# Kernel optimization log

Measured on AMD Instinct MI355X. Metric: run time of the kernel, lower is better.

The kernel has to match this reference:

```python
import jax, jax.numpy as jnp
import numpy as np

BN_EPS = 1e-5


def _bn(x, gamma, beta):
    # x: [B, C, L]; training-mode BatchNorm1d: biased stats over (B, L) per channel.
    mu = x.mean(axis=(0, 2), keepdims=True)
    var = x.var(axis=(0, 2), keepdims=True)
    return (x - mu) * jax.lax.rsqrt(var + BN_EPS) * gamma[None, :, None] + beta[None, :, None]


def _sblock(x, g1, be1, w1, bi1, g2, be2, w2, bi2):
    # x: [B, m, n] (n == m). bn1 over channel dim n after transpose.
    t = jnp.swapaxes(x, -2, -1)                      # [B, n, m]
    t = jax.nn.relu(_bn(t, g1, be1))
    t = jnp.einsum('bnm,km->bnk', t, w1) + bi1       # Linear(n,n) on last dim
    t = jnp.swapaxes(t, -2, -1)                      # [B, m, n]
    t = jax.nn.relu(_bn(t, g2, be2))                 # bn2 over channel dim m
    t = jnp.einsum('bmn,kn->bmk', t, w2) + bi2       # Linear(m,m) on last dim
    return t


def _forward(x, bn1_gamma, bn1_beta, w1, b1, bn2_gamma, bn2_beta, w2, b2):
    out = x
    num_blocks = w1.shape[0]
    for l in range(num_blocks):
        out = _sblock(out, bn1_gamma[l], bn1_beta[l], w1[l], b1[l],
                      bn2_gamma[l], bn2_beta[l], w2[l], b2[l])
    n, m = out.shape[-2], out.shape[-1]

    # greedy argmax row/col masking on a detached copy (batch index 0, as in torch)
    oc0 = jax.lax.stop_gradient(out[0])              # [n, m]
    neg_inf = jnp.float32(-jnp.inf)

    def body(line, state):
        oc, visited, mask = state
        idx = jnp.argmax(oc)
        i, j = idx // m, idx % m
        visited = visited.at[i].set(1.0)
        mask = mask.at[:, j].set(1.0 - visited)
        oc = oc.at[:, j].set(neg_inf)
        oc = oc.at[i, :].set(neg_inf)
        return oc, visited, mask

    init = (oc0, jnp.zeros((n,), jnp.float32), jnp.zeros((n, m), jnp.float32))
    _, _, mask = jax.lax.fori_loop(0, n, body, init)

    out = jnp.where(mask.astype(bool)[None], neg_inf, out)
    return jax.nn.softmax(out, axis=-1)


def setup_inputs() -> dict:
    key = jax.random.key(0)
    ks = jax.random.split(key, 9)
    L, n, m = 2, 2048, 2048
    return {
        'x': jax.random.normal(ks[0], (1, m, n), jnp.float32),
        'bn1_gamma': jax.random.uniform(ks[1], (L, n), jnp.float32, 0.5, 1.5),
        'bn1_beta': 0.1 * jax.random.normal(ks[2], (L, n), jnp.float32),
        'w1': 0.02 * jax.random.normal(ks[3], (L, n, n), jnp.float32),
        'b1': 0.02 * jax.random.normal(ks[4], (L, n), jnp.float32),
        'bn2_gamma': jax.random.uniform(ks[5], (L, m), jnp.float32, 0.5, 1.5),
        'bn2_beta': 0.1 * jax.random.normal(ks[6], (L, m), jnp.float32),
        'w2': 0.02 * jax.random.normal(ks[7], (L, m, m), jnp.float32),
        'b2': 0.02 * jax.random.normal(ks[8], (L, m), jnp.float32),
    }


def reference(x, bn1_gamma, bn1_beta, w1, b1, bn2_gamma, bn2_beta, w2, b2):
    return _forward(x, bn1_gamma, bn1_beta, w1, b1, bn2_gamma, bn2_beta, w2, b2)
```

## Files before the change

### kernel.cpp

```cpp
#include <hip/hip_runtime.h>
#include <math.h>

#define NEG_INF (-__builtin_inf())

typedef unsigned long long u64;

constexpr int N = 2048;
constexpr int NCHUNK = 32;
constexpr int RPC = N / NCHUNK;
constexpr int K_LIST = 64;
constexpr int BCAND = 128;
constexpr int CMAX = 256;
constexpr int CTGT = 96;

template<typename T> struct Key;
template<> struct Key<float>{
  static __device__ inline u64 pack(float x){
    unsigned u = __float_as_uint(x);
    u = (u & 0x80000000u) ? ~u : (u | 0x80000000u);
    return ((u64)u) << 32;
  }
};
template<> struct Key<double>{
  static __device__ inline u64 pack(double x){
    u64 u = (u64)__double_as_longlong(x);
    return (u >> 63) ? ~u : (u | 0x8000000000000000ull);
  }
};

__device__ inline bool kbetter(u64 k, unsigned rc, u64 bk, unsigned brc){
  return (k > bk) || (k == bk && rc < brc);
}

template<typename T>
__global__ __launch_bounds__(256) void colstats_partial(const T* __restrict__ X, double* __restrict__ part){
  int col = blockIdx.x * 256 + threadIdx.x;
  int r0  = blockIdx.y * RPC;
  double s = 0.0, q = 0.0;
  for (int r = r0; r < r0 + RPC; ++r){
    double v = (double)X[(size_t)r * N + col];
    s += v; q += v * v;
  }
  size_t o = (size_t)blockIdx.y * N + col;
  part[o*2+0] = s; part[o*2+1] = q;
}

__global__ __launch_bounds__(256) void colstats_final(const double* __restrict__ part,
    const float* __restrict__ g, const float* __restrict__ be,
    double* __restrict__ A, double* __restrict__ C){
  int col = blockIdx.x * 256 + threadIdx.x;
  double s = 0.0, q = 0.0;
  for (int k = 0; k < NCHUNK; ++k){
    size_t o = (size_t)k * N + col;
    s += part[o*2+0]; q += part[o*2+1];
  }
  double mu  = s / (double)N;
  double var = q / (double)N - mu * mu;
  double inv = 1.0 / sqrt(var + 1e-5);
  double a = (double)g[col] * inv;
  A[col] = a;
  C[col] = (double)be[col] - mu * a;
}

template<typename T>
__global__ __launch_bounds__(256) void rowstats(const T* __restrict__ Z,
    const float* __restrict__ g, const float* __restrict__ be,
    double* __restrict__ A, double* __restrict__ C){
  __shared__ double s1[256], s2[256];
  int r = blockIdx.x, tx = threadIdx.x;
  double s = 0.0, q = 0.0;
  for (int j = tx; j < N; j += 256){
    double v = (double)Z[(size_t)r * N + j];
    s += v; q += v * v;
  }
  s1[tx] = s; s2[tx] = q; __syncthreads();
  for (int st = 128; st; st >>= 1){
    if (tx < st){ s1[tx] += s1[tx + st]; s2[tx] += s2[tx + st]; }
    __syncthreads();
  }
  if (tx == 0){
    double mu  = s1[0] / (double)N;
    double var = s2[0] / (double)N - mu * mu;
    double inv = 1.0 / sqrt(var + 1e-5);
    double a = (double)g[r] * inv;
    A[r] = a;
    C[r] = (double)be[r] - mu * a;
  }
}

template<typename Tin, typename Tout>
__global__ __launch_bounds__(256) void bnrelu_col(const Tin* __restrict__ X,
    const double* __restrict__ A, const double* __restrict__ C, Tout* __restrict__ O){
  int i = blockIdx.x;
  for (int j = threadIdx.x; j < N; j += 256){
    double v = fma((double)X[(size_t)i * N + j], A[j], C[j]);
    O[(size_t)i * N + j] = (Tout)(v > 0.0 ? v : 0.0);
  }
}

template<typename Tin, typename Tout>
__global__ __launch_bounds__(256) void bnrelu_row(const Tin* __restrict__ Z,
    const double* __restrict__ A, const double* __restrict__ C, Tout* __restrict__ O){
  int i = blockIdx.x;
  double a = A[i], c = C[i];
  for (int j = threadIdx.x; j < N; j += 256){
    double v = fma((double)Z[(size_t)i * N + j], a, c);
    O[(size_t)i * N + j] = (Tout)(v > 0.0 ? v : 0.0);
  }
}

template<typename TA, typename TB, typename TO, typename TACC, bool BT, bool BIAS_ROW>
__global__ __launch_bounds__(256) void gemm_t(const TA* __restrict__ A, const TB* __restrict__ B,
    const float* __restrict__ bias, TO* __restrict__ O){
  __shared__ TACC sA[16][68];
  __shared__ TACC sB[16][68];
  const int tid = threadIdx.x;
  const int tx = tid & 15, ty = tid >> 4;
  const int i0 = blockIdx.y * 64, j0 = blockIdx.x * 64;
  TACC acc[4][4] = {};
  for (int k0 = 0; k0 < N; k0 += 16){
    {
      int r = tid >> 2, c4 = (tid & 3) * 4;
      const TA* p = A + (size_t)(i0 + r) * N + k0 + c4;
      TACC v0 = (TACC)p[0], v1 = (TACC)p[1], v2 = (TACC)p[2], v3 = (TACC)p[3];
      sA[c4+0][r] = v0; sA[c4+1][r] = v1; sA[c4+2][r] = v2; sA[c4+3][r] = v3;
    }
    if (!BT){
      int k = tid >> 4, j4 = (tid & 15) * 4;
      const TB* p = B + (size_t)(k0 + k) * N + j0 + j4;
      sB[k][j4+0] = (TACC)p[0]; sB[k][j4+1] = (TACC)p[1];
      sB[k][j4+2] = (TACC)p[2]; sB[k][j4+3] = (TACC)p[3];
    } else {
      int j = tid >> 2, c4 = (tid & 3) * 4;
      const TB* p = B + (size_t)(j0 + j) * N + k0 + c4;
      TACC v0 = (TACC)p[0], v1 = (TACC)p[1], v2 = (TACC)p[2], v3 = (TACC)p[3];
      sB[c4+0][j] = v0; sB[c4+1][j] = v1; sB[c4+2][j] = v2; sB[c4+3][j] = v3;
    }
    __syncthreads();
    #pragma unroll
    for (int kk = 0; kk < 16; ++kk){
      TACC a_[4], b_[4];
      #pragma unroll
      for (int q = 0; q < 4; ++q){ a_[q] = sA[kk][ty*4+q]; b_[q] = sB[kk][tx*4+q]; }
      #pragma unroll
      for (int mi = 0; mi < 4; ++mi)
        #pragma unroll
        for (int ni = 0; ni < 4; ++ni)
          acc[mi][ni] = fma(a_[mi], b_[ni], acc[mi][ni]);
    }
    __syncthreads();
  }
  #pragma unroll
  for (int mi = 0; mi < 4; ++mi){
    int i = i0 + ty*4 + mi;
    #pragma unroll
    for (int ni = 0; ni < 4; ++ni){
      int j = j0 + tx*4 + ni;
      TACC bv = BIAS_ROW ? (TACC)bias[i] : (TACC)bias[j];
      O[(size_t)i * N + j] = (TO)(acc[mi][ni] + bv);
    }
  }
}

template<typename T>
__global__ __launch_bounds__(256) void build_lists(const T* __restrict__ O,
    ulonglong2* __restrict__ list, unsigned short* __restrict__ llen,
    u64* __restrict__ rvK_g, unsigned* __restrict__ rvRC_g){
  __shared__ unsigned hist4[4][256];
  __shared__ unsigned hsum[256];
  __shared__ u64 candK[BCAND];
  __shared__ unsigned candRC[BCAND];
  __shared__ u64 redK[256];
  __shared__ unsigned redC[256];
  __shared__ u64 sTau;
  __shared__ unsigned sBstar, sPre, sDone, sC;
  const int r = blockIdx.x;
  const int tid = threadIdx.x;
  const int wave = tid >> 6, lane = tid & 63;
  const unsigned BIG = 0xFFFFFFFFu;
  const T* __restrict__ row = O + (size_t)r * N;
  const unsigned target = K_LIST;

  u64 base = 0; unsigned pre = 0; int shift = 56;
  for (int level = 0; level < 8; ++level){
    for (int i = tid; i < 4*256; i += 256) ((unsigned*)hist4)[i] = 0;
    __syncthreads();
    for (int c = tid; c < N; c += 256){
      u64 k = Key<T>::pack(row[c]);
      if (k >= base && ((k - base) >> shift) < 256)
        atomicAdd(&hist4[wave][(unsigned)((k - base) >> shift)], 1u);
    }
    __syncthreads();
    if (tid < 256) hsum[tid] = hist4[0][tid] + hist4[1][tid] + hist4[2][tid] + hist4[3][tid];
    __syncthreads();
    if (wave == 0){
      unsigned v0 = hsum[4*lane+0], v1 = hsum[4*lane+1], v2 = hsum[4*lane+2], v3 = hsum[4*lane+3];
      unsigned s3 = v3, s2 = v2+v3, s1 = v1+s2, tot = v0+s1;
      unsigned run = tot;
      #pragma unroll
      for (int off = 1; off < 64; off <<= 1){
        unsigned x = __shfl_down(run, off);
        if (lane + off < 64) run += x;
      }
      unsigned above = run - tot;
      unsigned ge0 = tot + above, ge1 = s1 + above, ge2 = s2 + above, ge3 = s3 + above;
      int bl = -1; unsigned geb = 0, vb = 0;
      if (pre + ge3 >= target){ bl = 4*lane+3; geb = ge3; vb = v3; }
      else if (pre + ge2 >= target){ bl = 4*lane+2; geb = ge2; vb = v2; }
      else if (pre + ge1 >= target){ bl = 4*lane+1; geb = ge1; vb = v1; }
      else if (pre + ge0 >= target){ bl = 4*lane+0; geb = ge0; vb = v0; }
      int bmax = bl;
      #pragma unroll
      for (int off = 32; off; off >>= 1){
        int o = __shfl_xor(bmax, off);
        if (o > bmax) bmax = o;
      }
      if (bmax < 0){
        if (lane == 0){ sBstar = 0; sPre = pre; sDone = 1; }
      } else if (bl == bmax){
        unsigned total = pre + geb;
        sBstar = (unsigned)bmax; sPre = pre + geb - vb;
        sDone = (total <= BCAND || shift == 0) ? 1u : 0u;
      }
    }
    __syncthreads();
    unsigned bstar = sBstar;
    if (sDone){
      if (tid == 0) sTau = base + ((u64)bstar << shift);
      break;
    }
    base += ((u64)bstar << shift);
    pre = sPre;
    shift -= 8;
    __syncthreads();
  }
  __syncthreads();
  const u64 tau = sTau;

  if (tid == 0) sC = 0;
  __syncthreads();
  for (int c = tid; c < N; c += 256){
    u64 k = Key<T>::pack(row[c]);
    if (k >= tau){
      unsigned p = atomicAdd(&sC, 1u);
      if (p < BCAND){ candK[p] = k; candRC[p] = ((unsigned)r << 11) | (unsigned)c; }
    }
  }
  __syncthreads();
  unsigned C = sC;

  if (C > BCAND){
    u64 bk = 0; unsigned bc = BIG;
    for (int c = tid; c < N; c += 256){
      u64 k = Key<T>::pack(row[c]);
      if (k > bk){ bk = k; bc = (unsigned)c; }
    }
    redK[tid] = bk; redC[tid] = bc; __syncthreads();
    for (int st = 128; st; st >>= 1){
      if (tid < st && kbetter(redK[tid+st], redC[tid+st], redK[tid], redC[tid])){
        redK[tid] = redK[tid+st]; redC[tid] = redC[tid+st];
      }
      __syncthreads();
    }
    if (tid == 0){
      llen[r] = 0;
      rvK_g[r] = redK[0];
      rvRC_g[r] = ((unsigned)r << 11) | (redC[0] & 2047u);
    }
    return;
  }

  unsigned S = 64; while (S < C) S <<= 1;
  for (unsigned p = C + tid; p < S; p += 256){ candK[p] = 0; candRC[p] = BIG; }
  __syncthreads();
  for (unsigned k2 = 2; k2 <= S; k2 <<= 1){
    for (unsigned jj = k2 >> 1; jj > 0; jj >>= 1){
      if (tid < (int)(S >> 1)){
        unsigned i = (((unsigned)tid & ~(jj - 1)) << 1) | ((unsigned)tid & (jj - 1));
        unsigned l = i | jj;
        bool up = ((i & k2) == 0);
        u64 ki = candK[i], kl = candK[l];
        unsigned ri = candRC[i], rl = candRC[l];
        bool lBeforeI = (kl > ki) || (kl == ki && rl < ri);
        bool iBeforeL = (ki > kl) || (ki == kl && ri < rl);
        if (up ? lBeforeI : iBeforeL){
          candK[i] = kl; candK[l] = ki; candRC[i] = rl; candRC[l] = ri;
        }
      }
      __syncthreads();
    }
  }

  unsigned outLen = (C < (unsigned)K_LIST) ? C : (unsigned)K_LIST;
  if (tid < (int)outLen){
    ulonglong2 e; e.x = candK[tid]; e.y = (u64)candRC[tid];
    list[(size_t)r * K_LIST + tid] = e;
  }
  if (tid == 0){
    llen[r] = (unsigned short)outLen;
    rvK_g[r] = candK[0];
    rvRC_g[r] = candRC[0];
  }
}

template<typename T>
__global__ __launch_bounds__(512) void greedy7(const T* __restrict__ O,
    const ulonglong2* __restrict__ list, const unsigned short* __restrict__ llen_g,
    const u64* __restrict__ rvK_g, const unsigned* __restrict__ rvRC_g,
    unsigned* __restrict__ rowStep_g, unsigned* __restrict__ colStep_g){
  __shared__ u64 rvK[N];
  __shared__ unsigned rvRC[N];
  __shared__ unsigned cm32[N/32];
  __shared__ unsigned short hIdx[N];
  __shared__ unsigned short hLen[N];
  __shared__ unsigned rowStepL[N];
  __shared__ unsigned colStepL[N];
  __shared__ unsigned hist[8][256];
  __shared__ unsigned hsum[256];
  __shared__ u64 candK[CMAX];
  __shared__ unsigned candRC[CMAX];
  __shared__ u64 sortK[CMAX];
  __shared__ unsigned sortRC[CMAX];
  __shared__ unsigned foc[N];
  __shared__ u64 redK8[8];
  __shared__ unsigned redC8[8];
  __shared__ u64 sTau;
  __shared__ unsigned sBstar, sPre, sDone, sC, sCnt, sL;
  const int tid  = threadIdx.x;
  const int lane = tid & 63, wave = tid >> 6;
  const unsigned BIG = 0xFFFFFFFFu;
  const u64 lmask = ((u64)1 << lane) - 1;

  for (int i = tid; i < N; i += 512){
    rvK[i] = rvK_g[i]; rvRC[i] = rvRC_g[i];
    unsigned short L0 = llen_g[i];
    hLen[i] = L0;
    hIdx[i] = (L0 == 0) ? (unsigned short)0xFFFFu : (unsigned short)1;
  }
  if (tid < N/32) cm32[tid] = 0xFFFFFFFFu;
  __syncthreads();

  unsigned t = 0;
  for (int rd = 0; rd < N && t < N; ++rd){
    const unsigned alive = N - t;
    const unsigned target = (alive < (unsigned)CTGT) ? alive : (unsigned)CTGT;
    if (tid == 0){ sC = 0; sCnt = 0; sL = BIG; }

    u64 base = 0; unsigned pre = 0; int shift = 56;
    for (int level = 0; level < 8; ++level){
      for (int i = tid; i < 8*256; i += 512) ((unsigned*)hist)[i] = 0;
      __syncthreads();
      #pragma unroll
      for (int rep = 0; rep < 4; ++rep){
        u64 k = rvK[rep*512 + tid];
        if (k >= base && k && ((k - base) >> shift) < 256)
          atomicAdd(&hist[wave][(unsigned)((k - base) >> shift)], 1u);
      }
      __syncthreads();
      if (tid < 256){
        unsigned s = 0;
        #pragma unroll
        for (int w = 0; w < 8; ++w) s += hist[w][tid];
        hsum[tid] = s;
      }
      __syncthreads();
      if (wave == 0){
        unsigned v0 = hsum[4*lane+0], v1 = hsum[4*lane+1], v2 = hsum[4*lane+2], v3 = hsum[4*lane+3];
        unsigned s3 = v3, s2 = v2+v3, s1 = v1+s2, tot = v0+s1;
        unsigned run = tot;
        #pragma unroll
        for (int off = 1; off < 64; off <<= 1){
          unsigned x = __shfl_down(run, off);
          if (lane + off < 64) run += x;
        }
        unsigned above = run - tot;
        unsigned ge0 = tot + above, ge1 = s1 + above, ge2 = s2 + above, ge3 = s3 + above;
        int bl = -1; unsigned geb = 0, vb = 0;
        if (pre + ge3 >= target){ bl = 4*lane+3; geb = ge3; vb = v3; }
        else if (pre + ge2 >= target){ bl = 4*lane+2; geb = ge2; vb = v2; }
        else if (pre + ge1 >= target){ bl = 4*lane+1; geb = ge1; vb = v1; }
        else if (pre + ge0 >= target){ bl = 4*lane+0; geb = ge0; vb = v0; }
        int bmax = bl;
        #pragma unroll
        for (int off = 32; off; off >>= 1){
          int o = __shfl_xor(bmax, off);
          if (o > bmax) bmax = o;
        }
        if (bmax < 0){
          if (lane == 0){ sBstar = 0; sPre = pre; sDone = 1; }
        } else if (bl == bmax){
          unsigned total = pre + geb;
          sBstar = (unsigned)bmax; sPre = pre + geb - vb;
          sDone = (total <= CMAX || shift == 0) ? 1u : 0u;
        }
      }
      __syncthreads();
      unsigned bstar = sBstar;
      if (sDone){
        if (tid == 0) sTau = base + ((u64)bstar << shift);
        break;
      }
      base += ((u64)bstar << shift);
      pre = sPre;
      shift -= 8;
      __syncthreads();
    }
    __syncthreads();
    const u64 tau = sTau;

    #pragma unroll
    for (int rep = 0; rep < 4; ++rep){
      int i = rep*512 + tid;
      u64 k = rvK[i];
      bool p = (k != 0) && (k >= tau);
      u64 m = __ballot(p);
      unsigned b = 0;
      if (lane == 0) b = atomicAdd(&sC, (unsigned)__popcll(m));
      b = __shfl(b, 0);
      if (p){
        unsigned pos = b + (unsigned)__popcll(m & lmask);
        if (pos < (unsigned)CMAX){ candK[pos] = k; candRC[pos] = rvRC[i]; }
      }
    }
    __syncthreads();
    const unsigned C = sC;

    unsigned L;
    if (C > (unsigned)CMAX){
      u64 bk = 0; unsigned brc = BIG;
      for (int i = tid; i < N; i += 512){
        u64 k = rvK[i];
        if (k && kbetter(k, rvRC[i], bk, brc)){ bk = k; brc = rvRC[i]; }
      }
      #pragma unroll
      for (int off = 32; off; off >>= 1){
        u64 ok = __shfl_xor(bk, off);
        unsigned oc = __shfl_xor(brc, off);
        if (kbetter(ok, oc, bk, brc)){ bk = ok; brc = oc; }
      }
      if (lane == 0){ redK8[wave] = bk; redC8[wave] = brc; }
      __syncthreads();
      if (tid == 0){
        u64 fk = redK8[0]; unsigned fc = redC8[0];
        for (int w = 1; w < 8; ++w)
          if (kbetter(redK8[w], redC8[w], fk, fc)){ fk = redK8[w]; fc = redC8[w]; }
        sortK[0] = fk; sortRC[0] = fc;
      }
      __syncthreads();
      L = 1;
    } else {
      if (tid < (int)C){
        u64 mk = candK[tid]; unsigned mrc = candRC[tid];
        unsigned rank = 0;
        for (unsigned j = 0; j < C; ++j)
          if (kbetter(candK[j], candRC[j], mk, mrc)) ++rank;
        sortK[rank] = mk; sortRC[rank] = mrc;
      }
      __syncthreads();
      if (tid < (int)C) foc[sortRC[tid] & 2047u] = BIG;
      __syncthreads();
      if (tid < (int)C) atomicMin(&foc[sortRC[tid] & 2047u], (unsigned)tid);
      __syncthreads();
      if (tid < (int)C && foc[sortRC[tid] & 2047u] < (unsigned)tid)
        atomicMin(&sL, (unsigned)tid);
      __syncthreads();
      L = (sL < C) ? sL : C;
    }

    if (tid < (int)L){
      unsigned rc = sortRC[tid];
      unsigned r = rc >> 11, c = rc & 2047u;
      rowStepL[r] = t + (unsigned)tid;
      colStepL[c] = t + (unsigned)tid;
      rvK[r] = 0;
      atomicAnd(&cm32[c >> 5], ~(1u << (c & 31)));
    }
    __syncthreads();
    t += L;
    if (t >= N) break;

    #pragma unroll
    for (int rep = 0; rep < 4; ++rep){
      int rr = rep*512 + tid;
      u64 k = rvK[rr];
      if (k == 0) continue;
      unsigned cc = rvRC[rr] & 2047u;
      if ((cm32[cc >> 5] >> (cc & 31)) & 1u) continue;
      unsigned hi = hIdx[rr];
      u64 nk = 0; unsigned nrc = 0;
      if (hi != 0xFFFFu){
        unsigned ln = hLen[rr];
        while (hi < ln){
          ulonglong2 e = list[(size_t)rr * K_LIST + hi];
          ++hi;
          unsigned ec = ((unsigned)e.y) & 2047u;
          if ((cm32[ec >> 5] >> (ec & 31)) & 1u){ nk = e.x; nrc = (unsigned)e.y; break; }
        }
      }
      if (nk){
        rvK[rr] = nk; rvRC[rr] = nrc; hIdx[rr] = (unsigned short)hi;
      } else {
        hIdx[rr] = (unsigned short)0xFFFFu;
        foc[atomicAdd(&sCnt, 1u)] = (unsigned)rr;
      }
    }
    __syncthreads();

    {
      const unsigned cnt = sCnt;
      for (unsigned q = (unsigned)wave; q < cnt; q += 8){
        unsigned rr = foc[q];
        const T* __restrict__ rowp = O + (size_t)rr * N;
        u64 bk = 0; unsigned bc = BIG;
        #pragma unroll
        for (int it = 0; it < N/64; ++it){
          int cc = lane + it*64;
          u64 kk = Key<T>::pack(rowp[cc]);
          if (!((cm32[cc >> 5] >> (cc & 31)) & 1u)) kk = 0;
          if (kbetter(kk, (unsigned)cc, bk, bc)){ bk = kk; bc = (unsigned)cc; }
        }
        #pragma unroll
        for (int off = 32; off; off >>= 1){
          u64 ok = __shfl_xor(bk, off);
          unsigned oc = __shfl_xor(bc, off);
          if (kbetter(ok, oc, bk, bc)){ bk = ok; bc = oc; }
        }
        if (lane == 0){ rvK[rr] = bk; rvRC[rr] = (rr << 11) | (bc & 2047u); }
      }
    }
    __syncthreads();
  }

  __syncthreads();
  for (int i = tid; i < N; i += 512){
    rowStep_g[i] = rowStepL[i];
    colStep_g[i] = colStepL[i];
  }
}

template<typename T>
__global__ __launch_bounds__(256) void masked_softmax(const T* __restrict__ O,
    const unsigned* __restrict__ rowStep, const unsigned* __restrict__ colStep,
    float* __restrict__ out){
  __shared__ double vals[N];
  __shared__ double red[256];
  int r = blockIdx.x, tx = threadIdx.x;
  unsigned s = rowStep[r];
  double mx = NEG_INF;
  for (int c = tx; c < N; c += 256){
    double v = (colStep[c] >= s) ? (double)O[(size_t)r * N + c] : NEG_INF;
    vals[c] = v;
    if (v > mx) mx = v;
  }
  red[tx] = mx; __syncthreads();
  for (int st = 128; st; st >>= 1){
    if (tx < st) red[tx] = fmax(red[tx], red[tx + st]);
    __syncthreads();
  }
  mx = red[0]; __syncthreads();
  double sm = 0.0;
  for (int c = tx; c < N; c += 256){
    double v = vals[c];
    double e = (v != NEG_INF) ? exp(v - mx) : 0.0;
    vals[c] = e;
    sm += e;
  }
  red[tx] = sm; __syncthreads();
  for (int st = 128; st; st >>= 1){
    if (tx < st) red[tx] += red[tx + st];
    __syncthreads();
  }
  double inv = 1.0 / red[0];
  for (int c = tx; c < N; c += 256){
    out[(size_t)r * N + c] = (float)(vals[c] * inv);
  }
}

template<typename T>
static void run_pipeline(const float* x, const float* g1, const float* be1,
                         const float* W1, const float* bi1,
                         const float* g2, const float* be2,
                         const float* W2, const float* bi2,
                         float* out, T* buf0, T* buf1,
                         double* part, double* stA, double* stC,
                         u64* rvK, unsigned* rvRC,
                         unsigned* rowStep, unsigned* colStep,
                         ulonglong2* list, unsigned short* llen,
                         hipStream_t s){
  dim3 gs(N/256, NCHUNK);
  dim3 gg(N/64, N/64);
  colstats_partial<float><<<gs,256,0,s>>>(x, part);
  colstats_final<<<N/256,256,0,s>>>(part, g1, be1, stA, stC);
  bnrelu_col<float,T><<<N,256,0,s>>>(x, stA, stC, buf0);
  gemm_t<float,T,T,T,false,true><<<gg,256,0,s>>>(W1, buf0, bi1, buf1);
  rowstats<T><<<N,256,0,s>>>(buf1, g2, be2, stA, stC);
  bnrelu_row<T,T><<<N,256,0,s>>>(buf1, stA, stC, buf0);
  gemm_t<T,float,T,T,true,false><<<gg,256,0,s>>>(buf0, W2, bi2, buf1);
  colstats_partial<T><<<gs,256,0,s>>>(buf1, part);
  colstats_final<<<N/256,256,0,s>>>(part, g1+N, be1+N, stA, stC);
  bnrelu_col<T,T><<<N,256,0,s>>>(buf1, stA, stC, buf0);
  gemm_t<float,T,T,T,false,true><<<gg,256,0,s>>>(W1+(size_t)N*N, buf0, bi1+N, buf1);
  rowstats<T><<<N,256,0,s>>>(buf1, g2+N, be2+N, stA, stC);
  bnrelu_row<T,T><<<N,256,0,s>>>(buf1, stA, stC, buf0);
  gemm_t<T,float,T,T,true,false><<<gg,256,0,s>>>(buf0, W2+(size_t)N*N, bi2+N, buf1);
  build_lists<T><<<N,256,0,s>>>(buf1, list, llen, rvK, rvRC);
  greedy7<T><<<1,512,0,s>>>(buf1, list, llen, rvK, rvRC, rowStep, colStep);
  masked_softmax<T><<<N,256,0,s>>>(buf1, rowStep, colStep, out);
}

extern "C" void kernel_launch(void* const* d_in, const int* in_sizes, int n_in,
                              void* d_out, int out_size, void* d_ws, size_t ws_size,
                              hipStream_t stream){
  if (n_in < 9) return;
  const float* x   = (const float*)d_in[0];
  const float* g1  = (const float*)d_in[1];
  const float* be1 = (const float*)d_in[2];
  const float* W1  = (const float*)d_in[3];
  const float* bi1 = (const float*)d_in[4];
  const float* g2  = (const float*)d_in[5];
  const float* be2 = (const float*)d_in[6];
  const float* W2  = (const float*)d_in[7];
  const float* bi2 = (const float*)d_in[8];
  float* out = (float*)d_out;

  char* base = (char*)d_ws;
  size_t off = 0;
  auto carve = [&](size_t bytes)->void*{
    void* q = base + off;
    off = (off + bytes + 255) & ~(size_t)255;
    return q;
  };
  double*   part    = (double*)carve((size_t)NCHUNK * N * 2 * sizeof(double));
  double*   stA     = (double*)carve(N * sizeof(double));
  double*   stC     = (double*)carve(N * sizeof(double));
  u64*      rvK     = (u64*)carve(N * sizeof(u64));
  unsigned* rvRC    = (unsigned*)carve(N * sizeof(unsigned));
  unsigned* rowStep = (unsigned*)carve(N * sizeof(unsigned));
  unsigned* colStep = (unsigned*)carve(N * sizeof(unsigned));
  ulonglong2* list  = (ulonglong2*)carve((size_t)N * K_LIST * sizeof(ulonglong2));
  unsigned short* llen = (unsigned short*)carve(N * sizeof(unsigned short));
  size_t smallEnd = off;

  const size_t matF = (size_t)N * N * sizeof(float);
  size_t needF  = smallEnd + 2 * (matF + 256);
  size_t needF1 = smallEnd + 1 * (matF + 256);

  if (ws_size >= needF){
    float* b0 = (float*)carve(matF);
    float* b1 = (float*)carve(matF);
    run_pipeline<float>(x,g1,be1,W1,bi1,g2,be2,W2,bi2, out, b0, b1,
                        part, stA, stC, rvK, rvRC, rowStep, colStep, list, llen, stream);
  } else if (ws_size >= needF1){
    float* b0 = (float*)carve(matF);
    float* b1 = out;
    run_pipeline<float>(x,g1,be1,W1,bi1,g2,be2,W2,bi2, out, b0, b1,
                        part, stA, stC, rvK, rvRC, rowStep, colStep, list, llen, stream);
  }
}
```

Measured before the change: 4.706 ms.

## Keep candidate pool across greedy rounds, rerun radix select only when pool runs low

The single-block greedy matching kernel used to run a full multi-level radix threshold search over all 2048 row maxima every round. It now keeps the sorted candidates that still sit above the previous threshold and whose row value did not change, carries them into the next round, and reruns the radix select only when that pool drops below a minimum size. The radix target is raised so each select yields a larger pool. This is meant to cut the per-round histogram and synchronisation cost in the serial greedy loop. The trade-offs are a larger rank sort per round and added complexity around when pooled candidates remain valid.

```diff
diff --git a/kernel.cpp b/kernel.cpp
--- a/kernel.cpp
+++ b/kernel.cpp
@@ -11,7 +11,8 @@
 constexpr int K_LIST = 64;
 constexpr int BCAND = 128;
 constexpr int CMAX = 256;
-constexpr int CTGT = 96;
+constexpr int CTGT = 240;
+constexpr int POOL_MIN = 48;
 
 template<typename T> struct Key;
 template<> struct Key<float>{
@@ -304,7 +305,7 @@
 }
 
 template<typename T>
-__global__ __launch_bounds__(512) void greedy7(const T* __restrict__ O,
+__global__ __launch_bounds__(512) void greedy9(const T* __restrict__ O,
     const ulonglong2* __restrict__ list, const unsigned short* __restrict__ llen_g,
     const u64* __restrict__ rvK_g, const unsigned* __restrict__ rvRC_g,
     unsigned* __restrict__ rowStep_g, unsigned* __restrict__ colStep_g){
@@ -324,8 +325,8 @@
   __shared__ unsigned foc[N];
   __shared__ u64 redK8[8];
   __shared__ unsigned redC8[8];
-  __shared__ u64 sTau;
-  __shared__ unsigned sBstar, sPre, sDone, sC, sCnt, sL;
+  __shared__ u64 sTau, sTauP;
+  __shared__ unsigned sBstar, sPre, sDone, sC, sCnt, sL, sPC;
   const int tid  = threadIdx.x;
   const int lane = tid & 63, wave = tid >> 6;
   const unsigned BIG = 0xFFFFFFFFu;
@@ -338,95 +339,109 @@
     hIdx[i] = (L0 == 0) ? (unsigned short)0xFFFFu : (unsigned short)1;
   }
   if (tid < N/32) cm32[tid] = 0xFFFFFFFFu;
+  if (tid == 0){ sPC = 0; sTauP = 0; }
   __syncthreads();
 
   unsigned t = 0;
   for (int rd = 0; rd < N && t < N; ++rd){
     const unsigned alive = N - t;
-    const unsigned target = (alive < (unsigned)CTGT) ? alive : (unsigned)CTGT;
-    if (tid == 0){ sC = 0; sCnt = 0; sL = BIG; }
-
-    u64 base = 0; unsigned pre = 0; int shift = 56;
-    for (int level = 0; level < 8; ++level){
-      for (int i = tid; i < 8*256; i += 512) ((unsigned*)hist)[i] = 0;
-      __syncthreads();
+    const unsigned PCin = sPC;
+    const bool needRadix = (PCin < (unsigned)POOL_MIN) && (PCin < alive);
+    if (tid == 0){ sCnt = 0; sL = BIG; }
+
+    unsigned PC;
+    u64 tau;
+    bool overflow = false;
+
+    if (needRadix){
+      const unsigned target = (alive < (unsigned)CTGT) ? alive : (unsigned)CTGT;
+      u64 base = 0; unsigned pre = 0; int shift = 56;
+      for (int level = 0; level < 8; ++level){
+        for (int i = tid; i < 8*256; i += 512) ((unsigned*)hist)[i] = 0;
+        __syncthreads();
+        #pragma unroll
+        for (int rep = 0; rep < 4; ++rep){
+          u64 k = rvK[rep*512 + tid];
+          if (k >= base && k && ((k - base) >> shift) < 256)
+            atomicAdd(&hist[wave][(unsigned)((k - base) >> shift)], 1u);
+        }
+        __syncthreads();
+        if (tid < 256){
+          unsigned s = 0;
+          #pragma unroll
+          for (int w = 0; w < 8; ++w) s += hist[w][tid];
+          hsum[tid] = s;
+        }
+        __syncthreads();
+        if (wave == 0){
+          unsigned v0 = hsum[4*lane+0], v1 = hsum[4*lane+1], v2 = hsum[4*lane+2], v3 = hsum[4*lane+3];
+          unsigned s3 = v3, s2 = v2+v3, s1 = v1+s2, tot = v0+s1;
+          unsigned run = tot;
+          #pragma unroll
+          for (int off = 1; off < 64; off <<= 1){
+            unsigned x = __shfl_down(run, off);
+            if (lane + off < 64) run += x;
+          }
+          unsigned above = run - tot;
+          unsigned ge0 = tot + above, ge1 = s1 + above, ge2 = s2 + above, ge3 = s3 + above;
+          int bl = -1; unsigned geb = 0, vb = 0;
+          if (pre + ge3 >= target){ bl = 4*lane+3; geb = ge3; vb = v3; }
+          else if (pre + ge2 >= target){ bl = 4*lane+2; geb = ge2; vb = v2; }
+          else if (pre + ge1 >= target){ bl = 4*lane+1; geb = ge1; vb = v1; }
+          else if (pre + ge0 >= target){ bl = 4*lane+0; geb = ge0; vb = v0; }
+          int bmax = bl;
+          #pragma unroll
+          for (int off = 32; off; off >>= 1){
+            int o = __shfl_xor(bmax, off);
+            if (o > bmax) bmax = o;
+          }
+          if (bmax < 0){
+            if (lane == 0){ sBstar = 0; sPre = pre; sDone = 1; }
+          } else if (bl == bmax){
+            unsigned total = pre + geb;
+            sBstar = (unsigned)bmax; sPre = pre + geb - vb;
+            sDone = (total <= CMAX || shift == 0) ? 1u : 0u;
+          }
+        }
+        __syncthreads();
+        unsigned bstar = sBstar;
+        if (sDone){
+          if (tid == 0){ sTau = base + ((u64)bstar << shift); sC = 0; }
+          break;
+        }
+        base += ((u64)bstar << shift);
+        pre = sPre;
+        shift -= 8;
+        __syncthreads();
+      }
+      __syncthreads();
+      tau = sTau;
+
       #pragma unroll
       for (int rep = 0; rep < 4; ++rep){
-        u64 k = rvK[rep*512 + tid];
-        if (k >= base && k && ((k - base) >> shift) < 256)
-          atomicAdd(&hist[wave][(unsigned)((k - base) >> shift)], 1u);
-      }
-      __syncthreads();
-      if (tid < 256){
-        unsigned s = 0;
-        #pragma unroll
-        for (int w = 0; w < 8; ++w) s += hist[w][tid];
-        hsum[tid] = s;
-      }
-      __syncthreads();
-      if (wave == 0){
-        unsigned v0 = hsum[4*lane+0], v1 = hsum[4*lane+1], v2 = hsum[4*lane+2], v3 = hsum[4*lane+3];
-        unsigned s3 = v3, s2 = v2+v3, s1 = v1+s2, tot = v0+s1;
-        unsigned run = tot;
-        #pragma unroll
-        for (int off = 1; off < 64; off <<= 1){
-          unsigned x = __shfl_down(run, off);
-          if (lane + off < 64) run += x;
-        }
-        unsigned above = run - tot;
-        unsigned ge0 = tot + above, ge1 = s1 + above, ge2 = s2 + above, ge3 = s3 + above;
-        int bl = -1; unsigned geb = 0, vb = 0;
-        if (pre + ge3 >= target){ bl = 4*lane+3; geb = ge3; vb = v3; }
-        else if (pre + ge2 >= target){ bl = 4*lane+2; geb = ge2; vb = v2; }
-        else if (pre + ge1 >= target){ bl = 4*lane+1; geb = ge1; vb = v1; }
-        else if (pre + ge0 >= target){ bl = 4*lane+0; geb = ge0; vb = v0; }
-        int bmax = bl;
-        #pragma unroll
-        for (int off = 32; off; off >>= 1){
-          int o = __shfl_xor(bmax, off);
-          if (o > bmax) bmax = o;
-        }
-        if (bmax < 0){
-          if (lane == 0){ sBstar = 0; sPre = pre; sDone = 1; }
-        } else if (bl == bmax){
-          unsigned total = pre + geb;
-          sBstar = (unsigned)bmax; sPre = pre + geb - vb;
-          sDone = (total <= CMAX || shift == 0) ? 1u : 0u;
-        }
-      }
-      __syncthreads();
-      unsigned bstar = sBstar;
-      if (sDone){
-        if (tid == 0) sTau = base + ((u64)bstar << shift);
-        break;
-      }
-      base += ((u64)bstar << shift);
-      pre = sPre;
-      shift -= 8;
-      __syncthreads();
-    }
-    __syncthreads();
-    const u64 tau = sTau;
-
-    #pragma unroll
-    for (int rep = 0; rep < 4; ++rep){
-      int i = rep*512 + tid;
-      u64 k = rvK[i];
-      bool p = (k != 0) && (k >= tau);
-      u64 m = __ballot(p);
-      unsigned b = 0;
-      if (lane == 0) b = atomicAdd(&sC, (unsigned)__popcll(m));
-      b = __shfl(b, 0);
-      if (p){
-        unsigned pos = b + (unsigned)__popcll(m & lmask);
-        if (pos < (unsigned)CMAX){ candK[pos] = k; candRC[pos] = rvRC[i]; }
-      }
-    }
-    __syncthreads();
-    const unsigned C = sC;
+        int i = rep*512 + tid;
+        u64 k = rvK[i];
+        bool p = (k != 0) && (k >= tau);
+        u64 m = __ballot(p);
+        unsigned b = 0;
+        if (lane == 0) b = atomicAdd(&sC, (unsigned)__popcll(m));
+        b = __shfl(b, 0);
+        if (p){
+          unsigned pos = b + (unsigned)__popcll(m & lmask);
+          if (pos < (unsigned)CMAX){ candK[pos] = k; candRC[pos] = rvRC[i]; }
+        }
+      }
+      __syncthreads();
+      PC = sC;
+      if (tid == 0) sTauP = tau;
+      overflow = (PC > (unsigned)CMAX);
+    } else {
+      PC = PCin;
+      tau = sTauP;
+    }
 
     unsigned L;
-    if (C > (unsigned)CMAX){
+    if (overflow){
       u64 bk = 0; unsigned brc = BIG;
       for (int i = tid; i < N; i += 512){
         u64 k = rvK[i];
@@ -449,22 +464,22 @@
       __syncthreads();
       L = 1;
     } else {
-      if (tid < (int)C){
+      if (tid < (int)PC){
         u64 mk = candK[tid]; unsigned mrc = candRC[tid];
         unsigned rank = 0;
-        for (unsigned j = 0; j < C; ++j)
+        for (unsigned j = 0; j < PC; ++j)
           if (kbetter(candK[j], candRC[j], mk, mrc)) ++rank;
         sortK[rank] = mk; sortRC[rank] = mrc;
       }
       __syncthreads();
-      if (tid < (int)C) foc[sortRC[tid] & 2047u] = BIG;
-      __syncthreads();
-      if (tid < (int)C) atomicMin(&foc[sortRC[tid] & 2047u], (unsigned)tid);
-      __syncthreads();
-      if (tid < (int)C && foc[sortRC[tid] & 2047u] < (unsigned)tid)
+      if (tid < (int)PC) foc[sortRC[tid] & 2047u] = BIG;
+      __syncthreads();
+      if (tid < (int)PC) atomicMin(&foc[sortRC[tid] & 2047u], (unsigned)tid);
+      __syncthreads();
+      if (tid < (int)PC && foc[sortRC[tid] & 2047u] < (unsigned)tid)
         atomicMin(&sL, (unsigned)tid);
       __syncthreads();
-      L = (sL < C) ? sL : C;
+      L = (sL < PC) ? sL : PC;
     }
 
     if (tid < (int)L){
@@ -527,6 +542,32 @@
         }
         if (lane == 0){ rvK[rr] = bk; rvRC[rr] = (rr << 11) | (bc & 2047u); }
       }
+    }
+    __syncthreads();
+
+    if (!overflow){
+      if (tid == 0) sC = 0;
+      __syncthreads();
+      unsigned p = L + (unsigned)tid;
+      u64 k = 0; unsigned rr = 0;
+      bool keep = false;
+      if (p < PC){
+        rr = sortRC[p] >> 11;
+        k = rvK[rr];
+        keep = (k != 0) && (k >= tau);
+      }
+      u64 m = __ballot(keep);
+      unsigned b = 0;
+      if (lane == 0) b = atomicAdd(&sC, (unsigned)__popcll(m));
+      b = __shfl(b, 0);
+      if (keep){
+        unsigned pos = b + (unsigned)__popcll(m & lmask);
+        candK[pos] = k; candRC[pos] = rvRC[rr];
+      }
+      __syncthreads();
+      if (tid == 0) sPC = sC;
+    } else {
+      if (tid == 0) sPC = 0;
     }
     __syncthreads();
   }
@@ -604,7 +645,7 @@
   bnrelu_row<T,T><<<N,256,0,s>>>(buf1, stA, stC, buf0);
   gemm_t<T,float,T,T,true,false><<<gg,256,0,s>>>(buf0, W2+(size_t)N*N, bi2+N, buf1);
   build_lists<T><<<N,256,0,s>>>(buf1, list, llen, rvK, rvRC);
-  greedy7<T><<<1,512,0,s>>>(buf1, list, llen, rvK, rvRC, rowStep, colStep);
+  greedy9<T><<<1,512,0,s>>>(buf1, list, llen, rvK, rvRC, rowStep, colStep);
   masked_softmax<T><<<N,256,0,s>>>(buf1, rowStep, colStep, out);
 }
 
```

New measurement: 4.556 ms. 1.03x faster.

## Replace radix-select threshold with sampled sort threshold in greedy kernel

Applied to the files above, without the earlier changes.

The single-block greedy matching kernel no longer runs a multi-level histogram radix select each round to find the candidate threshold. Instead, one wave samples 64 row-best keys, bitonic-sorts them with shuffles, and takes a high-rank sample as the threshold, retrying once with a stricter sample if too many candidates pass. The duplicate-column detection that used several barrier-separated phases with a shared array is folded into the rank computation. The aim is fewer barriers and shared-memory passes per round, at the cost of variable candidate counts and possibly more rounds or fallbacks to the single-max path.

```diff
diff --git a/kernel.cpp b/kernel.cpp
--- a/kernel.cpp
+++ b/kernel.cpp
@@ -10,8 +10,8 @@
 constexpr int RPC = N / NCHUNK;
 constexpr int K_LIST = 64;
 constexpr int BCAND = 128;
-constexpr int CMAX = 256;
-constexpr int CTGT = 96;
+constexpr int CMAX = 384;
+constexpr int SRANK = 4;
 
 template<typename T> struct Key;
 template<> struct Key<float>{
@@ -30,6 +30,23 @@
 
 __device__ inline bool kbetter(u64 k, unsigned rc, u64 bk, unsigned brc){
   return (k > bk) || (k == bk && rc < brc);
+}
+
+__device__ inline void sort64_desc(u64& k, unsigned& rc, int lane){
+  #pragma unroll
+  for (unsigned k2 = 2; k2 <= 64; k2 <<= 1){
+    #pragma unroll
+    for (unsigned j = 64; j; j >>= 1){
+      if (j > (k2 >> 1)) continue;
+      u64 ok = __shfl_xor(k, (int)j);
+      unsigned orc = __shfl_xor(rc, (int)j);
+      bool dirDesc = ((lane & k2) == 0);
+      bool lower   = ((lane & j) == 0);
+      bool takeOther = (dirDesc == lower) ? kbetter(ok, orc, k, rc)
+                                          : kbetter(k, rc, ok, orc);
+      if (takeOther){ k = ok; rc = orc; }
+    }
+  }
 }
 
 template<typename T>
@@ -304,7 +321,7 @@
 }
 
 template<typename T>
-__global__ __launch_bounds__(512) void greedy7(const T* __restrict__ O,
+__global__ __launch_bounds__(512) void greedy10(const T* __restrict__ O,
     const ulonglong2* __restrict__ list, const unsigned short* __restrict__ llen_g,
     const u64* __restrict__ rvK_g, const unsigned* __restrict__ rvRC_g,
     unsigned* __restrict__ rowStep_g, unsigned* __restrict__ colStep_g){
@@ -315,8 +332,6 @@
   __shared__ unsigned short hLen[N];
   __shared__ unsigned rowStepL[N];
   __shared__ unsigned colStepL[N];
-  __shared__ unsigned hist[8][256];
-  __shared__ unsigned hsum[256];
   __shared__ u64 candK[CMAX];
   __shared__ unsigned candRC[CMAX];
   __shared__ u64 sortK[CMAX];
@@ -324,8 +339,7 @@
   __shared__ unsigned foc[N];
   __shared__ u64 redK8[8];
   __shared__ unsigned redC8[8];
-  __shared__ u64 sTau;
-  __shared__ unsigned sBstar, sPre, sDone, sC, sCnt, sL;
+  __shared__ unsigned sC, sCnt, sL;
   const int tid  = threadIdx.x;
   const int lane = tid & 63, wave = tid >> 6;
   const unsigned BIG = 0xFFFFFFFFu;
@@ -338,75 +352,25 @@
     hIdx[i] = (L0 == 0) ? (unsigned short)0xFFFFu : (unsigned short)1;
   }
   if (tid < N/32) cm32[tid] = 0xFFFFFFFFu;
+  if (tid == 0){ sC = 0; sCnt = 0; sL = BIG; }
   __syncthreads();
 
   unsigned t = 0;
-  for (int rd = 0; rd < N && t < N; ++rd){
+  for (int rd = 0; rd < 4096 && t < N; ++rd){
     const unsigned alive = N - t;
-    const unsigned target = (alive < (unsigned)CTGT) ? alive : (unsigned)CTGT;
-    if (tid == 0){ sC = 0; sCnt = 0; sL = BIG; }
-
-    u64 base = 0; unsigned pre = 0; int shift = 56;
-    for (int level = 0; level < 8; ++level){
-      for (int i = tid; i < 8*256; i += 512) ((unsigned*)hist)[i] = 0;
-      __syncthreads();
-      #pragma unroll
-      for (int rep = 0; rep < 4; ++rep){
-        u64 k = rvK[rep*512 + tid];
-        if (k >= base && k && ((k - base) >> shift) < 256)
-          atomicAdd(&hist[wave][(unsigned)((k - base) >> shift)], 1u);
-      }
-      __syncthreads();
-      if (tid < 256){
-        unsigned s = 0;
-        #pragma unroll
-        for (int w = 0; w < 8; ++w) s += hist[w][tid];
-        hsum[tid] = s;
-      }
-      __syncthreads();
-      if (wave == 0){
-        unsigned v0 = hsum[4*lane+0], v1 = hsum[4*lane+1], v2 = hsum[4*lane+2], v3 = hsum[4*lane+3];
-        unsigned s3 = v3, s2 = v2+v3, s1 = v1+s2, tot = v0+s1;
-        unsigned run = tot;
-        #pragma unroll
-        for (int off = 1; off < 64; off <<= 1){
-          unsigned x = __shfl_down(run, off);
-          if (lane + off < 64) run += x;
-        }
-        unsigned above = run - tot;
-        unsigned ge0 = tot + above, ge1 = s1 + above, ge2 = s2 + above, ge3 = s3 + above;
-        int bl = -1; unsigned geb = 0, vb = 0;
-        if (pre + ge3 >= target){ bl = 4*lane+3; geb = ge3; vb = v3; }
-        else if (pre + ge2 >= target){ bl = 4*lane+2; geb = ge2; vb = v2; }
-        else if (pre + ge1 >= target){ bl = 4*lane+1; geb = ge1; vb = v1; }
-        else if (pre + ge0 >= target){ bl = 4*lane+0; geb = ge0; vb = v0; }
-        int bmax = bl;
-        #pragma unroll
-        for (int off = 32; off; off >>= 1){
-          int o = __shfl_xor(bmax, off);
-          if (o > bmax) bmax = o;
-        }
-        if (bmax < 0){
-          if (lane == 0){ sBstar = 0; sPre = pre; sDone = 1; }
-        } else if (bl == bmax){
-          unsigned total = pre + geb;
-          sBstar = (unsigned)bmax; sPre = pre + geb - vb;
-          sDone = (total <= CMAX || shift == 0) ? 1u : 0u;
-        }
-      }
-      __syncthreads();
-      unsigned bstar = sBstar;
-      if (sDone){
-        if (tid == 0) sTau = base + ((u64)bstar << shift);
-        break;
-      }
-      base += ((u64)bstar << shift);
-      pre = sPre;
-      shift -= 8;
-      __syncthreads();
-    }
-    __syncthreads();
-    const u64 tau = sTau;
+
+    u64 tau;
+    u64 skS = 0; unsigned srcS = (unsigned)lane;
+    bool sampled = false;
+    if (alive <= (unsigned)CMAX){
+      tau = 1;
+    } else {
+      skS = rvK[(lane*131 + rd*29) & 2047];
+      sort64_desc(skS, srcS, lane);
+      tau = __shfl(skS, SRANK);
+      if (tau == 0) tau = 1;
+      sampled = true;
+    }
 
     #pragma unroll
     for (int rep = 0; rep < 4; ++rep){
@@ -423,7 +387,33 @@
       }
     }
     __syncthreads();
-    const unsigned C = sC;
+    unsigned C = sC;
+
+    if (C > (unsigned)CMAX && sampled){
+      u64 tau2 = __shfl(skS, 1);
+      if (tau2 == 0) tau2 = 1;
+      if (tau2 != tau){
+        tau = tau2;
+        if (tid == 0) sC = 0;
+        __syncthreads();
+        #pragma unroll
+        for (int rep = 0; rep < 4; ++rep){
+          int i = rep*512 + tid;
+          u64 k = rvK[i];
+          bool p = (k != 0) && (k >= tau);
+          u64 m = __ballot(p);
+          unsigned b = 0;
+          if (lane == 0) b = atomicAdd(&sC, (unsigned)__popcll(m));
+          b = __shfl(b, 0);
+          if (p){
+            unsigned pos = b + (unsigned)__popcll(m & lmask);
+            if (pos < (unsigned)CMAX){ candK[pos] = k; candRC[pos] = rvRC[i]; }
+          }
+        }
+        __syncthreads();
+        C = sC;
+      }
+    }
 
     unsigned L;
     if (C > (unsigned)CMAX){
@@ -451,18 +441,17 @@
     } else {
       if (tid < (int)C){
         u64 mk = candK[tid]; unsigned mrc = candRC[tid];
-        unsigned rank = 0;
-        for (unsigned j = 0; j < C; ++j)
-          if (kbetter(candK[j], candRC[j], mk, mrc)) ++rank;
+        unsigned mcol = mrc & 2047u;
+        unsigned rank = 0; bool dup = false;
+        for (unsigned j = 0; j < C; ++j){
+          u64 kj = candK[j]; unsigned rj = candRC[j];
+          bool better = kbetter(kj, rj, mk, mrc);
+          rank += (unsigned)better;
+          dup |= (better && ((rj & 2047u) == mcol));
+        }
         sortK[rank] = mk; sortRC[rank] = mrc;
-      }
-      __syncthreads();
-      if (tid < (int)C) foc[sortRC[tid] & 2047u] = BIG;
-      __syncthreads();
-      if (tid < (int)C) atomicMin(&foc[sortRC[tid] & 2047u], (unsigned)tid);
-      __syncthreads();
-      if (tid < (int)C && foc[sortRC[tid] & 2047u] < (unsigned)tid)
-        atomicMin(&sL, (unsigned)tid);
+        if (dup) atomicMin(&sL, rank);
+      }
       __syncthreads();
       L = (sL < C) ? sL : C;
     }
@@ -528,6 +517,7 @@
         if (lane == 0){ rvK[rr] = bk; rvRC[rr] = (rr << 11) | (bc & 2047u); }
       }
     }
+    if (tid == 0){ sC = 0; sCnt = 0; sL = BIG; }
     __syncthreads();
   }
 
@@ -604,7 +594,7 @@
   bnrelu_row<T,T><<<N,256,0,s>>>(buf1, stA, stC, buf0);
   gemm_t<T,float,T,T,true,false><<<gg,256,0,s>>>(buf0, W2+(size_t)N*N, bi2+N, buf1);
   build_lists<T><<<N,256,0,s>>>(buf1, list, llen, rvK, rvRC);
-  greedy7<T><<<1,512,0,s>>>(buf1, list, llen, rvK, rvRC, rowStep, colStep);
+  greedy10<T><<<1,512,0,s>>>(buf1, list, llen, rvK, rvRC, rowStep, colStep);
   masked_softmax<T><<<N,256,0,s>>>(buf1, rowStep, colStep, out);
 }
 
```

Result: slower. 4.996 ms (+6.2%).
